# Performance work log

Measured on AMD Instinct MI355X. Metric: run time of the kernel, lower is better.

## Reference

```python
import jax, jax.numpy as jnp
import numpy as np

DIM_HEAD = 64
LN_EPS = 1e-6  # flax nn.LayerNorm default


def setup_inputs() -> dict:
    key = jax.random.key(0)
    ks = jax.random.split(key, 5)
    B, N, D, H, Dh = 4, 1024, 768, 12, 64
    x = jax.random.normal(ks[0], (B, N, D), dtype=jnp.float32)
    Wq = jax.random.normal(ks[1], (D, H, Dh), dtype=jnp.float32) * (1.0 / np.sqrt(D))
    Wk = jax.random.normal(ks[2], (D, H, Dh), dtype=jnp.float32) * (1.0 / np.sqrt(D))
    Wv = jax.random.normal(ks[3], (D, H, Dh), dtype=jnp.float32) * (1.0 / np.sqrt(D))
    theta = jax.random.normal(ks[4], (H, H), dtype=jnp.float32) * (1.0 / np.sqrt(H))
    ln_scale = jnp.ones((N,), dtype=jnp.float32)
    ln_bias = jnp.zeros((N,), dtype=jnp.float32)
    return {"x": x, "Wq": Wq, "Wk": Wk, "Wv": Wv, "theta": theta,
            "ln_scale": ln_scale, "ln_bias": ln_bias}


def reference(x, Wq, Wk, Wv, theta, ln_scale, ln_bias):
    # x: [B, N, D]; W*: [D, H, Dh]; theta: [H, H]; ln_*: [N]
    q = jnp.einsum('bnd,dhe->bnhe', x, Wq) / jnp.sqrt(jnp.float32(DIM_HEAD))
    k = jnp.einsum('bnd,dhe->bnhe', x, Wk)
    v = jnp.einsum('bnd,dhe->bnhe', x, Wv)
    # attention scores over key axis: [B, H, N, N]
    attn = jnp.einsum('bqhd,bkhd->bhqk', q, k)
    attn = jax.nn.softmax(attn, axis=-1)
    # cross-head theta mixing: 'h i, b h q k -> b i q k'
    attn = jnp.einsum('hi,bhqk->biqk', theta, attn)
    # LayerNorm over last (key) axis with learnable scale/bias of shape [N]
    mean = jnp.mean(attn, axis=-1, keepdims=True)
    var = jnp.mean(jnp.square(attn - mean), axis=-1, keepdims=True)
    attn = (attn - mean) * jax.lax.rsqrt(var + LN_EPS) * ln_scale + ln_bias
    # note: output indexed by k (as in the original source einsum)
    out = jnp.einsum('bhqk,bqhd->bkhd', attn, v)
    B, N, H, Dh = out.shape
    return out.reshape(B, N, H * Dh)
```

## Files before the change

### kernel.cpp

```cpp
#include <hip/hip_runtime.h>

#define NB    4
#define NSEQ  1024
#define DMODEL 768
#define NH    12
#define DH    64

typedef __bf16 bf16x8 __attribute__((ext_vector_type(8)));
typedef float  floatx4 __attribute__((ext_vector_type(4)));
typedef unsigned int u32;

static __device__ __forceinline__ float bf2f(unsigned short u) {
    return __uint_as_float(((unsigned)u) << 16);
}
static __device__ __forceinline__ unsigned short f2bf(float f) {
    unsigned u = __float_as_uint(f);
    u += 0x7FFFu + ((u >> 16) & 1u);
    return (unsigned short)(u >> 16);
}

static __device__ __forceinline__ void gl_lds16(const void* g, void* l) {
    __builtin_amdgcn_global_load_lds(
        (const __attribute__((address_space(1))) unsigned int*)g,
        (__attribute__((address_space(3))) unsigned int*)l, 16, 0, 0);
}

__global__ __launch_bounds__(256) void cast_x(
    const float* __restrict__ x, unsigned short* __restrict__ xb)
{
    const int g = blockIdx.x * 256 + threadIdx.x;
    const size_t base = (size_t)g * 8;
    float4 a = *(const float4*)(x + base);
    float4 b = *(const float4*)(x + base + 4);
    unsigned short o[8];
    o[0] = f2bf(a.x); o[1] = f2bf(a.y); o[2] = f2bf(a.z); o[3] = f2bf(a.w);
    o[4] = f2bf(b.x); o[5] = f2bf(b.y); o[6] = f2bf(b.z); o[7] = f2bf(b.w);
    *(uint4*)(xb + base) = *(uint4*)o;
}

__global__ __launch_bounds__(256) void tr_w(
    const float* __restrict__ Wq, const float* __restrict__ Wk,
    const float* __restrict__ Wv, unsigned short* __restrict__ Wt)
{
    const int z  = blockIdx.z;
    const float* __restrict__ W = (z == 0) ? Wq : (z == 1) ? Wk : Wv;
    const int c0 = blockIdx.x * 64;
    const int k0 = blockIdx.y * 64;
    const int t  = threadIdx.x;

    __shared__ float ls[64][65];

    const int lr = t >> 2;
    #pragma unroll
    for (int j = 0; j < 4; j++) {
        int col = (t & 3) * 16 + j * 4;
        float4 v = *(const float4*)(W + (size_t)(k0 + lr) * DMODEL + c0 + col);
        ls[lr][col + 0] = v.x; ls[lr][col + 1] = v.y;
        ls[lr][col + 2] = v.z; ls[lr][col + 3] = v.w;
    }
    __syncthreads();
    const int lc = t >> 2;
    #pragma unroll
    for (int j = 0; j < 4; j++) {
        int kb = (t & 3) * 16 + j * 4;
        ushort4 o;
        o.x = f2bf(ls[kb + 0][lc]); o.y = f2bf(ls[kb + 1][lc]);
        o.z = f2bf(ls[kb + 2][lc]); o.w = f2bf(ls[kb + 3][lc]);
        *(ushort4*)(Wt + (size_t)z * DMODEL * DMODEL + (size_t)(c0 + lc) * DMODEL + k0 + kb) = o;
    }
}

__global__ __launch_bounds__(256) void qkv_mfma(
    const unsigned short* __restrict__ xb, const unsigned short* __restrict__ Wt,
    unsigned short* __restrict__ Q, unsigned short* __restrict__ K,
    unsigned short* __restrict__ V)
{
    const int z  = blockIdx.z;
    const int r0 = blockIdx.x * 128;
    const int c0 = blockIdx.y * 128;
    const int t    = threadIdx.x;
    const int wave = t >> 6, lane = t & 63;
    const int m = lane & 15, g = lane >> 4;

    const unsigned short* __restrict__ B = Wt + (size_t)z * DMODEL * DMODEL;

    __shared__ __align__(16) char sm[34816];
    unsigned short (*As)[32] = (unsigned short(*)[32])sm;
    unsigned short (*Bs)[32] = (unsigned short(*)[32])(sm + 8192);
    unsigned short (*Po)[136] = (unsigned short(*)[136])sm;

    const int wm = (wave >> 1) * 64;
    const int wn = (wave & 1) * 64;

    floatx4 acc[4][4] = {};

    const unsigned short* ga0 = xb + (size_t)(r0 + (t >> 2)) * DMODEL + (t & 3) * 8;
    const unsigned short* ga1 = ga0 + (size_t)64 * DMODEL;
    const unsigned short* gb0 = B  + (size_t)(c0 + (t >> 2)) * DMODEL + (t & 3) * 8;
    const unsigned short* gb1 = gb0 + (size_t)64 * DMODEL;
    unsigned short* la0 = (unsigned short*)sm + (size_t)t * 8;
    unsigned short* la1 = la0 + 2048;
    unsigned short* lb0 = (unsigned short*)(sm + 8192) + (size_t)t * 8;
    unsigned short* lb1 = lb0 + 2048;

    for (int kk = 0; kk < DMODEL / 32; kk++) {
        gl_lds16(ga0 + kk * 32, la0);
        gl_lds16(ga1 + kk * 32, la1);
        gl_lds16(gb0 + kk * 32, lb0);
        gl_lds16(gb1 + kk * 32, lb1);
        __syncthreads();

        bf16x8 af[4], bf[4];
        #pragma unroll
        for (int mt = 0; mt < 4; mt++)
            af[mt] = *(const bf16x8*)&As[wm + mt * 16 + m][g * 8];
        #pragma unroll
        for (int nt = 0; nt < 4; nt++)
            bf[nt] = *(const bf16x8*)&Bs[wn + nt * 16 + m][g * 8];
        #pragma unroll
        for (int mt = 0; mt < 4; mt++)
            #pragma unroll
            for (int nt = 0; nt < 4; nt++)
                acc[mt][nt] = __builtin_amdgcn_mfma_f32_16x16x32_bf16(
                    af[mt], bf[nt], acc[mt][nt], 0, 0, 0);
        __syncthreads();
    }

    const float scale = (z == 0) ? 0.125f : 1.0f;
    #pragma unroll
    for (int mt = 0; mt < 4; mt++) {
        #pragma unroll
        for (int nt = 0; nt < 4; nt++) {
            int rloc = wm + mt * 16 + g * 4;
            int cloc = wn + nt * 16 + m;
            #pragma unroll
            for (int r = 0; r < 4; r++)
                Po[rloc + r][cloc] = f2bf(acc[mt][nt][r] * scale);
        }
    }
    __syncthreads();

    #pragma unroll
    for (int i = 0; i < 8; i++) {
        int ci = t + i * 256;
        int row = ci >> 4, off = (ci & 15) * 8;
        uint4 val = *(uint4*)&Po[row][off];
        if (z == 0) {
            *(uint4*)(Q + (size_t)(r0 + row) * DMODEL + c0 + off) = val;
        } else {
            unsigned short* Pp = (z == 1) ? K : V;
            int rr = r0 + row;
            int bb = rr >> 10, n = rr & 1023;
            int cc = c0 + off;
            int h = cc >> 6, d = cc & 63;
            *(uint4*)(Pp + (((size_t)bb * NH + h) * NSEQ + n) * DH + d) = val;
        }
    }
}

__global__ __launch_bounds__(256) void score_gemm(
    const unsigned short* __restrict__ Q, const unsigned short* __restrict__ K,
    unsigned short* __restrict__ P, float* __restrict__ Lpart)
{
    const int bh = blockIdx.z;
    const int b  = bh / NH, h = bh % NH;
    const int q0 = blockIdx.x * 128;
    const int k0 = blockIdx.y * 128;
    const int t    = threadIdx.x;
    const int wave = t >> 6, lane = t & 63;

    __shared__ __align__(16) char sm[36864];
    unsigned short (*Qs)[72] = (unsigned short(*)[72])sm;
    unsigned short (*Ks)[72] = (unsigned short(*)[72])(sm + 18432);
    unsigned short (*Po)[136] = (unsigned short(*)[136])sm;
    float (*rsum)[2] = (float(*)[2])(sm + 34816);

    #pragma unroll
    for (int i = 0; i < 4; i++) {
        int c = t + i * 256;
        int row = c >> 3, off = (c & 7) * 8;
        uint4 qa = *(const uint4*)(Q + ((size_t)(b * NSEQ + q0 + row)) * DMODEL + h * DH + off);
        uint4 ka = *(const uint4*)(K + (((size_t)bh) * NSEQ + (k0 + row)) * DH + off);
        *(uint4*)&Qs[row][off] = qa;
        *(uint4*)&Ks[row][off] = ka;
    }
    __syncthreads();

    const int wq = (wave >> 1) * 64, wk2 = (wave & 1) * 64;
    const int m = lane & 15, g = lane >> 4;

    floatx4 acc[4][4] = {};
    #pragma unroll
    for (int ds = 0; ds < 2; ds++) {
        const int dd = ds * 32 + g * 8;
        bf16x8 af[4], bf[4];
        #pragma unroll
        for (int mt = 0; mt < 4; mt++)
            af[mt] = *(const bf16x8*)&Qs[wq + mt * 16 + m][dd];
        #pragma unroll
        for (int nt = 0; nt < 4; nt++)
            bf[nt] = *(const bf16x8*)&Ks[wk2 + nt * 16 + m][dd];
        #pragma unroll
        for (int mt = 0; mt < 4; mt++)
            #pragma unroll
            for (int nt = 0; nt < 4; nt++)
                acc[mt][nt] = __builtin_amdgcn_mfma_f32_16x16x32_bf16(
                    af[mt], bf[nt], acc[mt][nt], 0, 0, 0);
    }

    __syncthreads();
    float rs[4][4] = {};
    #pragma unroll
    for (int mt = 0; mt < 4; mt++) {
        #pragma unroll
        for (int nt = 0; nt < 4; nt++) {
            int qloc = wq + mt * 16 + g * 4;
            int kloc = wk2 + nt * 16 + m;
            #pragma unroll
            for (int r = 0; r < 4; r++) {
                float e = __expf(acc[mt][nt][r]);
                Po[qloc + r][kloc] = f2bf(e);
                rs[mt][r] += e;
            }
        }
    }
    #pragma unroll
    for (int mt = 0; mt < 4; mt++)
        #pragma unroll
        for (int r = 0; r < 4; r++) {
            float x = rs[mt][r];
            #pragma unroll
            for (int off = 1; off < 16; off <<= 1)
                x += __shfl_xor(x, off, 64);
            rs[mt][r] = x;
        }
    if (m == 0) {
        #pragma unroll
        for (int mt = 0; mt < 4; mt++)
            #pragma unroll
            for (int r = 0; r < 4; r++)
                rsum[wq + mt * 16 + g * 4 + r][wk2 >> 6] = rs[mt][r];
    }
    __syncthreads();

    if (t < 128)
        Lpart[((size_t)bh * 8 + blockIdx.y) * NSEQ + q0 + t] = rsum[t][0] + rsum[t][1];

    #pragma unroll
    for (int i = 0; i < 8; i++) {
        int c = t + i * 256;
        int row = c >> 4, off = (c & 15) * 8;
        *(uint4*)(P + (((size_t)bh * NSEQ) + q0 + row) * NSEQ + k0 + off) =
            *(uint4*)&Po[row][off];
    }
}

__global__ __launch_bounds__(256) void mix_t(
    unsigned short* __restrict__ P, const float* __restrict__ theta,
    const float* __restrict__ Lpart, float* __restrict__ Rbuf)
{
    const int t = threadIdx.x;
    const int wave = t >> 6, lane = t & 63;
    const int q = blockIdx.x, b = blockIdx.y;
    const int k0 = t * 4;

    __shared__ float th_s[144];
    __shared__ float red[4][12];

    unsigned short* Pq = P + ((size_t)b * NH * NSEQ + q) * NSEQ;

    uint2 praw[12];
    #pragma unroll
    for (int h = 0; h < 12; h++)
        praw[h] = *(const uint2*)(Pq + (size_t)h * NSEQ * NSEQ + k0);

    if (t < 144) th_s[t] = theta[t];

    float rl = 0.f;
    if (lane < 12) {
        float s = 0.f;
        #pragma unroll
        for (int kt = 0; kt < 8; kt++)
            s += Lpart[(((size_t)(b * NH + lane)) * 8 + kt) * NSEQ + q];
        rl = 1.0f / s;
    }
    float rlv[12];
    #pragma unroll
    for (int h = 0; h < 12; h++) rlv[h] = __shfl(rl, h, 64);

    __syncthreads();

    float p[12][4];
    #pragma unroll
    for (int h = 0; h < 12; h++) {
        const unsigned short* u = (const unsigned short*)&praw[h];
        p[h][0] = bf2f(u[0]) * rlv[h];
        p[h][1] = bf2f(u[1]) * rlv[h];
        p[h][2] = bf2f(u[2]) * rlv[h];
        p[h][3] = bf2f(u[3]) * rlv[h];
    }

    float rs[12];
    #pragma unroll
    for (int i = 0; i < 12; i++) {
        float s0 = 0.f, s1 = 0.f, s2 = 0.f, s3 = 0.f;
        #pragma unroll
        for (int h = 0; h < 12; h++) {
            float th = th_s[h * 12 + i];
            s0 = fmaf(th, p[h][0], s0); s1 = fmaf(th, p[h][1], s1);
            s2 = fmaf(th, p[h][2], s2); s3 = fmaf(th, p[h][3], s3);
        }
        ushort4 o;
        o.x = f2bf(s0); o.y = f2bf(s1); o.z = f2bf(s2); o.w = f2bf(s3);
        *(ushort4*)(Pq + (size_t)i * NSEQ * NSEQ + k0) = o;
        rs[i] = fmaf(s0, s0, fmaf(s1, s1, fmaf(s2, s2, s3 * s3)));
    }

    #pragma unroll
    for (int i = 0; i < 12; i++) {
        float x = rs[i];
        #pragma unroll
        for (int off = 32; off > 0; off >>= 1)
            x += __shfl_xor(x, off, 64);
        rs[i] = x;
    }
    if (lane < 12) {
        float myrs = 0.f;
        #pragma unroll
        for (int i = 0; i < 12; i++)
            if (lane == i) myrs = rs[i];
        red[wave][lane] = myrs;
    }
    __syncthreads();
    if (t < 12) {
        float sum2 = red[0][t] + red[1][t] + red[2][t] + red[3][t];
        float mean = 0.f;
        #pragma unroll
        for (int h = 0; h < 12; h++) mean += th_s[h * 12 + t];
        mean *= (1.0f / 1024.0f);
        float var = sum2 * (1.0f / 1024.0f) - mean * mean;
        Rbuf[(size_t)(b * NH + t) * NSEQ + q] = rsqrtf(var + 1e-6f);
    }
}

__global__ __launch_bounds__(256) void av_mfma(
    const unsigned short* __restrict__ A, const unsigned short* __restrict__ V,
    const float* __restrict__ Rbuf, const float* __restrict__ theta,
    const float* __restrict__ ln_scale, const float* __restrict__ ln_bias,
    float* __restrict__ out)
{
    const int b  = blockIdx.z;
    const int i  = blockIdx.y;
    const int k0 = blockIdx.x * 64;
    const int t  = threadIdx.x;
    const int wave = t >> 6, lane = t & 63;
    const int m = lane & 15, g = lane >> 4;

    __shared__ __align__(16) u32 At[64 * 33 + 64];
    __shared__ __align__(16) u32 Vt[64 * 33 + 64];

    const unsigned short* Ai = A + ((size_t)(b * NH + i)) * NSEQ * NSEQ;
    const unsigned short* Vi = V + ((size_t)(b * NH + i)) * NSEQ * DH;
    const float* Rb = Rbuf + (size_t)(b * NH + i) * NSEQ;

    const int wk = (wave >> 1) * 32;
    const int wd = (wave & 1) * 32;

    floatx4 acc[2][2] = {};
    float c1[4] = {}, c2[4] = {};
    const int k4s = (t & 15) * 4;

    for (int q0 = 0; q0 < NSEQ; q0 += 64) {
        ushort4 a0[2], a1[2], v0[2], v1[2];
        float2 rr[2];
        #pragma unroll
        for (int l = 0; l < 2; l++) {
            int c = t + l * 256;
            int k4 = (c & 15) * 4;
            int qp = c >> 4;
            a0[l] = *(const ushort4*)(Ai + (size_t)(q0 + 2 * qp)     * NSEQ + k0 + k4);
            a1[l] = *(const ushort4*)(Ai + (size_t)(q0 + 2 * qp + 1) * NSEQ + k0 + k4);
            v0[l] = *(const ushort4*)(Vi + (size_t)(q0 + 2 * qp)     * DH + k4);
            v1[l] = *(const ushort4*)(Vi + (size_t)(q0 + 2 * qp + 1) * DH + k4);
            rr[l] = *(const float2*)(Rb + q0 + 2 * qp);
        }
        __syncthreads();
        #pragma unroll
        for (int l = 0; l < 2; l++) {
            int c = t + l * 256;
            int k4 = (c & 15) * 4;
            int qp = c >> 4;
            const unsigned short* pa0 = (const unsigned short*)&a0[l];
            const unsigned short* pa1 = (const unsigned short*)&a1[l];
            const unsigned short* pv0 = (const unsigned short*)&v0[l];
            const unsigned short* pv1 = (const unsigned short*)&v1[l];
            #pragma unroll
            for (int j = 0; j < 4; j++) {
                At[(k4 + j) * 33 + qp] = (u32)pa0[j] | ((u32)pa1[j] << 16);
                float vf0 = bf2f(pv0[j]), vf1 = bf2f(pv1[j]);
                float s0 = rr[l].x * vf0, s1 = rr[l].y * vf1;
                Vt[(k4 + j) * 33 + qp] = (u32)f2bf(s0) | ((u32)f2bf(s1) << 16);
                c1[j] += s0 + s1;
                c2[j] += vf0 + vf1;
            }
        }
        __syncthreads();

        #pragma unroll
        for (int ks = 0; ks < 2; ks++) {
            const int qo = ks * 16 + g * 4;
            bf16x8 af[2], bf[2];
            #pragma unroll
            for (int mt = 0; mt < 2; mt++) {
                const u32* r = &At[(wk + mt * 16 + m) * 33 + qo];
                uint4 w; w.x = r[0]; w.y = r[1]; w.z = r[2]; w.w = r[3];
                af[mt] = *(bf16x8*)&w;
            }
            #pragma unroll
            for (int nt = 0; nt < 2; nt++) {
                const u32* r = &Vt[(wd + nt * 16 + m) * 33 + qo];
                uint4 w; w.x = r[0]; w.y = r[1]; w.z = r[2]; w.w = r[3];
                bf[nt] = *(bf16x8*)&w;
            }
            #pragma unroll
            for (int mt = 0; mt < 2; mt++)
                #pragma unroll
                for (int nt = 0; nt < 2; nt++)
                    acc[mt][nt] = __builtin_amdgcn_mfma_f32_16x16x32_bf16(
                        af[mt], bf[nt], acc[mt][nt], 0, 0, 0);
        }
    }

    __syncthreads();
    float* c1l = (float*)At;
    float* c2l = (float*)Vt;
    const int grp = t >> 4;
    #pragma unroll
    for (int j = 0; j < 4; j++) {
        c1l[grp * 64 + k4s + j] = c1[j];
        c2l[grp * 64 + k4s + j] = c2[j];
    }
    __syncthreads();
    if (t < 64) {
        float s1_ = 0.f, s2_ = 0.f;
        #pragma unroll
        for (int g2 = 0; g2 < 16; g2++) {
            s1_ += c1l[g2 * 64 + t];
            s2_ += c2l[g2 * 64 + t];
        }
        c1l[1024 + t] = s1_;
        c2l[1024 + t] = s2_;
    }
    __syncthreads();

    float mean = 0.f;
    #pragma unroll
    for (int h = 0; h < 12; h++) mean += theta[h * 12 + i];
    mean *= (1.0f / 1024.0f);

    #pragma unroll
    for (int mt = 0; mt < 2; mt++) {
        int kb = k0 + wk + mt * 16 + g * 4;
        float4 ls4 = *(const float4*)(ln_scale + kb);
        float4 lb4 = *(const float4*)(ln_bias + kb);
        #pragma unroll
        for (int nt = 0; nt < 2; nt++) {
            int d = wd + nt * 16 + m;
            float C1d = c1l[1024 + d], C2d = c2l[1024 + d];
            #pragma unroll
            for (int r = 0; r < 4; r++) {
                float lns = (&ls4.x)[r], lnb = (&lb4.x)[r];
                float val = lns * (acc[mt][nt][r] - mean * C1d) + lnb * C2d;
                out[((size_t)(b * NSEQ + kb + r)) * DMODEL + i * DH + d] = val;
            }
        }
    }
}

extern "C" void kernel_launch(void* const* d_in, const int* in_sizes, int n_in,
                              void* d_out, int out_size, void* d_ws, size_t ws_size,
                              hipStream_t stream) {
    const float* x     = (const float*)d_in[0];
    const float* Wq    = (const float*)d_in[1];
    const float* Wk    = (const float*)d_in[2];
    const float* Wv    = (const float*)d_in[3];
    const float* theta = (const float*)d_in[4];
    const float* ln_s  = (const float*)d_in[5];
    const float* ln_b  = (const float*)d_in[6];
    float* out = (float*)d_out;

    char* ws = (char*)d_ws;
    const size_t qsz = (size_t)NB * NSEQ * DMODEL * sizeof(unsigned short);
    unsigned short* Q = (unsigned short*)(ws);
    unsigned short* K = (unsigned short*)(ws + qsz);
    unsigned short* V = (unsigned short*)(ws + 2 * qsz);
    unsigned short* P = (unsigned short*)(ws + 3 * qsz);
    unsigned short* xb = P;
    unsigned short* Wt = P + (size_t)NB * NSEQ * DMODEL;

    float* Lpart = out;
    float* Rbuf  = (float*)K;

    cast_x<<<dim3(NB * NSEQ * DMODEL / 2048), 256, 0, stream>>>(x, xb);
    tr_w<<<dim3(12, 12, 3), 256, 0, stream>>>(Wq, Wk, Wv, Wt);
    qkv_mfma<<<dim3(NB * NSEQ / 128, DMODEL / 128, 3), 256, 0, stream>>>(
        xb, Wt, Q, K, V);
    score_gemm<<<dim3(NSEQ / 128, NSEQ / 128, NB * NH), 256, 0, stream>>>(Q, K, P, Lpart);
    mix_t<<<dim3(NSEQ, NB), 256, 0, stream>>>(P, theta, Lpart, Rbuf);
    av_mfma<<<dim3(NSEQ / 64, NH, NB), 256, 0, stream>>>(
        P, V, Rbuf, theta, ln_s, ln_b, out);
}
```

Baseline: 209.1 us.

## Precompute rstd-scaled V and column sums in separate kernel before AV GEMM

Adds a scale_v kernel that multiplies V by the per-query LayerNorm rstd, writes the scaled bf16 V into a reused buffer, and computes the per-column sums C1/C2 once per (batch, head). Previously every av_mfma block, one per 64-key tile (16 per head), recomputed this scaling and these reductions redundantly. av_mfma now just packs V into LDS and sums four partial column sums at the epilogue. The score kernel also switches to the hardware bf16 conversion. The cost is an extra kernel launch and an extra pass over V through global memory.

```diff
diff --git a/kernel.cpp b/kernel.cpp
--- a/kernel.cpp
+++ b/kernel.cpp
@@ -7,6 +7,7 @@
 #define DH    64
 
 typedef __bf16 bf16x8 __attribute__((ext_vector_type(8)));
+typedef __bf16 bf16x4 __attribute__((ext_vector_type(4)));
 typedef float  floatx4 __attribute__((ext_vector_type(4)));
 typedef unsigned int u32;
 
@@ -17,6 +18,10 @@
     unsigned u = __float_as_uint(f);
     u += 0x7FFFu + ((u >> 16) & 1u);
     return (unsigned short)(u >> 16);
+}
+static __device__ __forceinline__ unsigned short f2bf_hw(float f) {
+    __bf16 b = (__bf16)f;
+    return *(unsigned short*)&b;
 }
 
 static __device__ __forceinline__ void gl_lds16(const void* g, void* l) {
@@ -219,7 +224,7 @@
             #pragma unroll
             for (int r = 0; r < 4; r++) {
                 float e = __expf(acc[mt][nt][r]);
-                Po[qloc + r][kloc] = f2bf(e);
+                Po[qloc + r][kloc] = f2bf_hw(e);
                 rs[mt][r] += e;
             }
         }
@@ -343,9 +348,60 @@
     }
 }
 
+__global__ __launch_bounds__(256) void scale_v(
+    const unsigned short* __restrict__ V, const float* __restrict__ Rbuf,
+    unsigned short* __restrict__ Vs, float* __restrict__ C1p,
+    float* __restrict__ C2p)
+{
+    const int qh = blockIdx.x;
+    const int bi = blockIdx.y;
+    const int t  = threadIdx.x;
+    const int d4 = (t & 15) * 4;
+    const int qg = t >> 4;
+
+    __shared__ float rl_s[256];
+    __shared__ float c1l[16][64], c2l[16][64];
+
+    const unsigned short* Vi = V  + (size_t)bi * NSEQ * DH + (size_t)qh * 256 * DH;
+    unsigned short*       Vo = Vs + (size_t)bi * NSEQ * DH + (size_t)qh * 256 * DH;
+    const float* Rb = Rbuf + (size_t)bi * NSEQ + qh * 256;
+
+    rl_s[t] = Rb[t];
+    __syncthreads();
+
+    float s1[4] = {}, s2[4] = {};
+    #pragma unroll
+    for (int qq = 0; qq < 16; qq++) {
+        int q = qg * 16 + qq;
+        ushort4 v = *(const ushort4*)(Vi + (size_t)q * DH + d4);
+        float r = rl_s[q];
+        float f0 = bf2f(v.x), f1 = bf2f(v.y), f2 = bf2f(v.z), f3 = bf2f(v.w);
+        float g0 = r * f0, g1 = r * f1, g2 = r * f2, g3 = r * f3;
+        ushort4 o;
+        o.x = f2bf_hw(g0); o.y = f2bf_hw(g1); o.z = f2bf_hw(g2); o.w = f2bf_hw(g3);
+        *(ushort4*)(Vo + (size_t)q * DH + d4) = o;
+        s1[0] += g0; s1[1] += g1; s1[2] += g2; s1[3] += g3;
+        s2[0] += f0; s2[1] += f1; s2[2] += f2; s2[3] += f3;
+    }
+    #pragma unroll
+    for (int j = 0; j < 4; j++) {
+        c1l[qg][d4 + j] = s1[j];
+        c2l[qg][d4 + j] = s2[j];
+    }
+    __syncthreads();
+    if (t < 64) {
+        float a = 0.f, c = 0.f;
+        #pragma unroll
+        for (int g2 = 0; g2 < 16; g2++) { a += c1l[g2][t]; c += c2l[g2][t]; }
+        C1p[((size_t)bi * 4 + qh) * 64 + t] = a;
+        C2p[((size_t)bi * 4 + qh) * 64 + t] = c;
+    }
+}
+
 __global__ __launch_bounds__(256) void av_mfma(
-    const unsigned short* __restrict__ A, const unsigned short* __restrict__ V,
-    const float* __restrict__ Rbuf, const float* __restrict__ theta,
+    const unsigned short* __restrict__ A, const unsigned short* __restrict__ Vs,
+    const float* __restrict__ C1p, const float* __restrict__ C2p,
+    const float* __restrict__ theta,
     const float* __restrict__ ln_scale, const float* __restrict__ ln_bias,
     float* __restrict__ out)
 {
@@ -356,23 +412,20 @@
     const int wave = t >> 6, lane = t & 63;
     const int m = lane & 15, g = lane >> 4;
 
-    __shared__ __align__(16) u32 At[64 * 33 + 64];
-    __shared__ __align__(16) u32 Vt[64 * 33 + 64];
-
-    const unsigned short* Ai = A + ((size_t)(b * NH + i)) * NSEQ * NSEQ;
-    const unsigned short* Vi = V + ((size_t)(b * NH + i)) * NSEQ * DH;
-    const float* Rb = Rbuf + (size_t)(b * NH + i) * NSEQ;
+    __shared__ __align__(16) u32 At[64 * 33];
+    __shared__ __align__(16) u32 Vt[64 * 33];
+
+    const int bi = b * NH + i;
+    const unsigned short* Ai = A  + (size_t)bi * NSEQ * NSEQ;
+    const unsigned short* Vi = Vs + (size_t)bi * NSEQ * DH;
 
     const int wk = (wave >> 1) * 32;
     const int wd = (wave & 1) * 32;
 
     floatx4 acc[2][2] = {};
-    float c1[4] = {}, c2[4] = {};
-    const int k4s = (t & 15) * 4;
 
     for (int q0 = 0; q0 < NSEQ; q0 += 64) {
         ushort4 a0[2], a1[2], v0[2], v1[2];
-        float2 rr[2];
         #pragma unroll
         for (int l = 0; l < 2; l++) {
             int c = t + l * 256;
@@ -382,7 +435,6 @@
             a1[l] = *(const ushort4*)(Ai + (size_t)(q0 + 2 * qp + 1) * NSEQ + k0 + k4);
             v0[l] = *(const ushort4*)(Vi + (size_t)(q0 + 2 * qp)     * DH + k4);
             v1[l] = *(const ushort4*)(Vi + (size_t)(q0 + 2 * qp + 1) * DH + k4);
-            rr[l] = *(const float2*)(Rb + q0 + 2 * qp);
         }
         __syncthreads();
         #pragma unroll
@@ -397,11 +449,7 @@
             #pragma unroll
             for (int j = 0; j < 4; j++) {
                 At[(k4 + j) * 33 + qp] = (u32)pa0[j] | ((u32)pa1[j] << 16);
-                float vf0 = bf2f(pv0[j]), vf1 = bf2f(pv1[j]);
-                float s0 = rr[l].x * vf0, s1 = rr[l].y * vf1;
-                Vt[(k4 + j) * 33 + qp] = (u32)f2bf(s0) | ((u32)f2bf(s1) << 16);
-                c1[j] += s0 + s1;
-                c2[j] += vf0 + vf1;
+                Vt[(k4 + j) * 33 + qp] = (u32)pv0[j] | ((u32)pv1[j] << 16);
             }
         }
         __syncthreads();
@@ -431,28 +479,6 @@
         }
     }
 
-    __syncthreads();
-    float* c1l = (float*)At;
-    float* c2l = (float*)Vt;
-    const int grp = t >> 4;
-    #pragma unroll
-    for (int j = 0; j < 4; j++) {
-        c1l[grp * 64 + k4s + j] = c1[j];
-        c2l[grp * 64 + k4s + j] = c2[j];
-    }
-    __syncthreads();
-    if (t < 64) {
-        float s1_ = 0.f, s2_ = 0.f;
-        #pragma unroll
-        for (int g2 = 0; g2 < 16; g2++) {
-            s1_ += c1l[g2 * 64 + t];
-            s2_ += c2l[g2 * 64 + t];
-        }
-        c1l[1024 + t] = s1_;
-        c2l[1024 + t] = s2_;
-    }
-    __syncthreads();
-
     float mean = 0.f;
     #pragma unroll
     for (int h = 0; h < 12; h++) mean += theta[h * 12 + i];
@@ -466,7 +492,12 @@
         #pragma unroll
         for (int nt = 0; nt < 2; nt++) {
             int d = wd + nt * 16 + m;
-            float C1d = c1l[1024 + d], C2d = c2l[1024 + d];
+            float C1d = 0.f, C2d = 0.f;
+            #pragma unroll
+            for (int p4 = 0; p4 < 4; p4++) {
+                C1d += C1p[((size_t)bi * 4 + p4) * 64 + d];
+                C2d += C2p[((size_t)bi * 4 + p4) * 64 + d];
+            }
             #pragma unroll
             for (int r = 0; r < 4; r++) {
                 float lns = (&ls4.x)[r], lnb = (&lb4.x)[r];
@@ -500,6 +531,9 @@
 
     float* Lpart = out;
     float* Rbuf  = (float*)K;
+    unsigned short* Vsb = Q;
+    float* C1p = (float*)(ws + qsz + (1u << 20));
+    float* C2p = (float*)(ws + qsz + (2u << 20));
 
     cast_x<<<dim3(NB * NSEQ * DMODEL / 2048), 256, 0, stream>>>(x, xb);
     tr_w<<<dim3(12, 12, 3), 256, 0, stream>>>(Wq, Wk, Wv, Wt);
@@ -507,6 +541,7 @@
         xb, Wt, Q, K, V);
     score_gemm<<<dim3(NSEQ / 128, NSEQ / 128, NB * NH), 256, 0, stream>>>(Q, K, P, Lpart);
     mix_t<<<dim3(NSEQ, NB), 256, 0, stream>>>(P, theta, Lpart, Rbuf);
+    scale_v<<<dim3(4, NB * NH), 256, 0, stream>>>(V, Rbuf, Vsb, C1p, C2p);
     av_mfma<<<dim3(NSEQ / 64, NH, NB), 256, 0, stream>>>(
-        P, V, Rbuf, theta, ln_s, ln_b, out);
-}
+        P, Vsb, C1p, C2p, theta, ln_s, ln_b, out);
+}
```

New measurement: 213.5 us. 1.02x slower.
